# Kernel optimization log

Measured on AMD Instinct MI355X. Metric: run time of the kernel, lower is better.

Reference implementation:

```python
import jax, jax.numpy as jnp
import numpy as np

N_NODES = 100_000
N_EDGES = 1_600_000
F_IN = 128
NHID = 128
G = 64            # num graphs in the batch
N_CLASSES = 2
EMB = NHID * 6    # embedding_data dim so concat dim == NHID*8


def _lin_init(k, fi, fo):
    s = 1.0 / np.sqrt(fi)
    k1, k2 = jax.random.split(k)
    w = jax.random.uniform(k1, (fi, fo), jnp.float32, -s, s)
    b = jax.random.uniform(k2, (fo,), jnp.float32, -s, s)
    return w, b


def setup_inputs() -> dict:
    key = jax.random.key(0)
    ks = jax.random.split(key, 12)
    x = jax.random.normal(ks[0], (N_NODES, F_IN), jnp.float32)
    edge_index = jax.random.randint(ks[1], (2, N_EDGES), 0, N_NODES, dtype=jnp.int32)
    per = N_NODES // G
    batch = jnp.minimum(jnp.arange(N_NODES, dtype=jnp.int32) // per, G - 1)  # sorted, even split
    embedding_data = jax.random.normal(ks[2], (G, EMB), jnp.float32)
    conv_w, conv_b = _lin_init(ks[3], F_IN, NHID)
    lin0_w, lin0_b = _lin_init(ks[4], F_IN, NHID)
    lin1_w, lin1_b = _lin_init(ks[5], NHID * 8, NHID * 4)
    lin2_w, lin2_b = _lin_init(ks[6], NHID * 4, NHID * 2)
    lin3_w, lin3_b = _lin_init(ks[7], NHID * 2, NHID)
    lin4_w, lin4_b = _lin_init(ks[8], NHID, N_CLASSES)
    return {
        "x": x, "embedding_data": embedding_data,
        "conv_w": conv_w, "conv_b": conv_b,
        "lin0_w": lin0_w, "lin0_b": lin0_b,
        "lin1_w": lin1_w, "lin1_b": lin1_b,
        "lin2_w": lin2_w, "lin2_b": lin2_b,
        "lin3_w": lin3_w, "lin3_b": lin3_b,
        "lin4_w": lin4_w, "lin4_b": lin4_b,
        "edge_index": edge_index, "batch": batch,
    }


def _gcn_conv(x, edge_index, w, b):
    """PyG GCNConv: add self-loops, symmetric deg^-1/2 normalization, linear, scatter-add."""
    n = x.shape[0]
    loop = jnp.arange(n, dtype=edge_index.dtype)
    src = jnp.concatenate([edge_index[0], loop])
    dst = jnp.concatenate([edge_index[1], loop])
    deg = jax.ops.segment_sum(jnp.ones_like(dst, dtype=x.dtype), dst, num_segments=n)
    dinv = jnp.where(deg > 0, jax.lax.rsqrt(deg), 0.0)
    norm = dinv[src] * dinv[dst]                     # [E+N]
    h = x @ w                                        # [N, NHID]
    msg = h[src] * norm[:, None]                     # gather  [E+N, NHID]
    out = jax.ops.segment_sum(msg, dst, num_segments=n)  # scatter-add
    return out + b


def reference(x, embedding_data, conv_w, conv_b, lin0_w, lin0_b,
              lin1_w, lin1_b, lin2_w, lin2_b, lin3_w, lin3_b,
              lin4_w, lin4_b, edge_index, batch):
    h = jax.nn.relu(_gcn_conv(x, edge_index, conv_w, conv_b))   # [N, NHID]
    pooled = jax.ops.segment_max(h, batch, num_segments=G)      # global max pool [G, NHID]
    # first node of each graph (batch is sorted)
    first_idx = jnp.searchsorted(batch, jnp.arange(G, dtype=batch.dtype))
    news = jax.nn.relu(x[first_idx] @ lin0_w + lin0_b)          # [G, NHID]
    z = jnp.concatenate([pooled, news, embedding_data], axis=1) # [G, NHID*8]
    z = jnp.tanh(z @ lin1_w + lin1_b)   # dropout = identity (eval mode)
    z = jnp.tanh(z @ lin2_w + lin2_b)
    z = jnp.tanh(z @ lin3_w + lin3_b)
    return jax.nn.log_softmax(z @ lin4_w + lin4_b, axis=-1)     # [G, N_CLASSES]
```

## Files before the change

kernel.cpp:

```cpp
#include <hip/hip_runtime.h>
#include <hip/hip_bf16.h>

#define N_NODES 100000
#define N_EDGES 1600000
#define F 128
#define G 64
#define EMB 768
#define PER 1562
#define CAP 96
#define NBUCK 256
#define BNODES 391
#define TILE 8192
#define NBIN 196
#define SLOT 80
#define GEMM_GRID 512
#define EWS_ENT 104

typedef __hip_bfloat16 bf16;
typedef __attribute__((ext_vector_type(8))) short short8;
typedef __attribute__((ext_vector_type(4))) float f32x4;
typedef unsigned int u32;

__device__ __forceinline__ float b2f(bf16 v) { return __bfloat162float(v); }
__device__ __forceinline__ short f2bs(float v) {
    bf16 b = __float2bfloat16(v);
    return *reinterpret_cast<short*>(&b);
}
__device__ __forceinline__ float bl16(u32 v) { return __uint_as_float(v << 16); }
__device__ __forceinline__ float bh16(u32 v) { return __uint_as_float(v & 0xffff0000u); }

__global__ void k_init(float* __restrict__ pooled) {
    int i = blockIdx.x * 256 + threadIdx.x;
    if (i < G * F) pooled[i] = 0.0f;
}

__global__ __launch_bounds__(256) void k_fat(const int* __restrict__ ei,
                                             int* __restrict__ cntarr,
                                             u32* __restrict__ stage,
                                             const float* __restrict__ x,
                                             const float* __restrict__ w,
                                             bf16* __restrict__ h) {
    int t = threadIdx.x;
    if (blockIdx.x < NBIN) {
        __shared__ int offs[NBUCK];
        offs[t] = 0;
        __syncthreads();
        int blk = blockIdx.x;
        int e0 = blk * TILE;
        int e1 = min(e0 + TILE, N_EDGES);
        for (int e = e0 + t; e < e1; e += 256) {
            int src = ei[e];
            int dst = ei[N_EDGES + e];
            int b = dst / BNODES;
            int dl = dst - b * BNODES;
            int pos = atomicAdd(&offs[b], 1);
            if (pos < SLOT)
                stage[((size_t)b * NBIN + blk) * SLOT + pos] = (u32)src | ((u32)dl << 17);
        }
        __syncthreads();
        cntarr[blk * NBUCK + t] = min(offs[t], SLOT);
    } else {
        __shared__ short wfrag[16384];
        for (int i = t; i < 16384; i += 256) {
            int j    = i & 7;
            int lane = (i >> 3) & 63;
            int kb   = (i >> 9) & 3;
            int ct   = i >> 11;
            int k    = kb * 32 + (lane >> 4) * 8 + j;
            int n    = ct * 16 + (lane & 15);
            wfrag[i] = f2bs(w[k * 128 + n]);
        }
        __syncthreads();

        int wv = t >> 6, lane = t & 63;
        int m = lane & 15, q = lane >> 4;
        int nchunks = (N_NODES + 63) / 64;
        for (int chunk = blockIdx.x - NBIN; chunk < nchunks; chunk += GEMM_GRID) {
            int row = chunk * 64 + wv * 16 + m;
            int rr = (row < N_NODES) ? row : 0;
            short8 a[4];
#pragma unroll
            for (int kb = 0; kb < 4; ++kb) {
                const float* src = x + (size_t)rr * F + kb * 32 + q * 8;
                float4 v0 = *(const float4*)src;
                float4 v1 = *(const float4*)(src + 4);
                short8 av;
                av[0] = f2bs(v0.x); av[1] = f2bs(v0.y); av[2] = f2bs(v0.z); av[3] = f2bs(v0.w);
                av[4] = f2bs(v1.x); av[5] = f2bs(v1.y); av[6] = f2bs(v1.z); av[7] = f2bs(v1.w);
                a[kb] = av;
            }
            f32x4 acc[8];
#pragma unroll
            for (int ct = 0; ct < 8; ++ct) {
                f32x4 c = {0.f, 0.f, 0.f, 0.f};
#pragma unroll
                for (int kb = 0; kb < 4; ++kb) {
                    short8 bfr = *(const short8*)&wfrag[((ct * 4 + kb) * 64 + lane) * 8];
                    c = __builtin_amdgcn_mfma_f32_16x16x32_bf16(a[kb], bfr, c, 0, 0, 0);
                }
                acc[ct] = c;
            }
            int rbase = chunk * 64 + wv * 16 + q * 4;
#pragma unroll
            for (int ct = 0; ct < 8; ++ct)
#pragma unroll
                for (int r = 0; r < 4; ++r) {
                    int ro = rbase + r;
                    if (ro < N_NODES) h[(size_t)ro * F + ct * 16 + m] = __float2bfloat16(acc[ct][r]);
                }
        }
    }
}

__global__ __launch_bounds__(1024) void k_scat(const u32* __restrict__ stage,
                                               const int* __restrict__ cntarr,
                                               int* __restrict__ cursor,
                                               float* __restrict__ dinv,
                                               int* __restrict__ slots) {
    __shared__ int lcur[BNODES];
    int b = blockIdx.x;
    int t = threadIdx.x;
    int wv = t >> 6, lane = t & 63;
    int nbase = b * BNODES;
    int bn = min(BNODES, N_NODES - nbase);
    if (bn <= 0) return;
    for (int l = t; l < bn; l += 1024) lcur[l] = 0;
    __syncthreads();
    for (int seg = wv; seg < NBIN; seg += 16) {
        int cnt = cntarr[seg * NBUCK + b];
        const u32* sp = stage + ((size_t)b * NBIN + seg) * SLOT;
        for (int i = lane; i < cnt; i += 64) {
            u32 p = sp[i];
            int src = (int)(p & 0x1FFFFu);
            int dl  = (int)(p >> 17);
            int pos = atomicAdd(&lcur[dl], 1);
            if (pos < CAP) slots[(size_t)(nbase + dl) * CAP + pos] = src;
        }
    }
    __syncthreads();
    for (int l = t; l < bn; l += 1024) {
        int c = lcur[l];
        cursor[nbase + l] = c;
        dinv[nbase + l] = rsqrtf((float)(c + 1));
    }
}

__global__ __launch_bounds__(256) void k_agg(const bf16* __restrict__ h,
                                             const float* __restrict__ dinv,
                                             const int* __restrict__ slots,
                                             const int* __restrict__ cnt,
                                             const float* __restrict__ cb,
                                             float* __restrict__ pooled) {
    __shared__ __align__(16) char smem[16 * EWS_ENT * 8];
    int2 (*ews)[EWS_ENT] = (int2(*)[EWS_ENT])smem;
    float (*red)[132] = (float(*)[132])smem;

    int t = threadIdx.x;
    int wv = t >> 6, lane = t & 63;
    int q  = lane >> 4;
    int fl = lane & 15;
    int nb = blockIdx.x * 16 + wv * 4;
    int node = nb + q;
    int row  = wv * 4 + q;

    int c0 = min(cnt[nb + 0], CAP), c1 = min(cnt[nb + 1], CAP);
    int c2 = min(cnt[nb + 2], CAP), c3 = min(cnt[nb + 3], CAP);
    int cq   = (q == 0) ? c0 : (q == 1) ? c1 : (q == 2) ? c2 : c3;
    int cmax = max(max(c0, c1), max(c2, c3));

    const int* slp = slots + (size_t)node * CAP;
#pragma unroll
    for (int k = 0; k < 7; ++k) {
        int j = k * 16 + fl;
        if (j < EWS_ENT) {
            int2 ew = {0, 0};
            if (j < cq) { int s = slp[j]; ew.x = s; ew.y = __float_as_int(dinv[s]); }
            ews[row][j] = ew;
        }
    }
    __syncthreads();

    float acc[8] = {0.f, 0.f, 0.f, 0.f, 0.f, 0.f, 0.f, 0.f};
    const uint4* ewv = (const uint4*)ews[row];
    const u32* hb = (const u32*)h;
    int fl4 = fl * 4;
    if (cmax > 0) {
        uint4 ea = ewv[0];
        uint4 eb = ewv[1];
        uint4 v0 = *(const uint4*)(hb + (size_t)ea.x * 64 + fl4);
        uint4 v1 = *(const uint4*)(hb + (size_t)ea.z * 64 + fl4);
        uint4 v2 = *(const uint4*)(hb + (size_t)eb.x * 64 + fl4);
        uint4 v3 = *(const uint4*)(hb + (size_t)eb.z * 64 + fl4);
        for (int s0 = 0; s0 < cmax; s0 += 4) {
            uint4 na = ewv[(s0 >> 1) + 2];
            uint4 nb4 = ewv[(s0 >> 1) + 3];
            uint4 n0 = *(const uint4*)(hb + (size_t)na.x * 64 + fl4);
            uint4 n1 = *(const uint4*)(hb + (size_t)na.z * 64 + fl4);
            uint4 n2 = *(const uint4*)(hb + (size_t)nb4.x * 64 + fl4);
            uint4 n3 = *(const uint4*)(hb + (size_t)nb4.z * 64 + fl4);
            float w0 = __uint_as_float(ea.y), w1 = __uint_as_float(ea.w);
            float w2 = __uint_as_float(eb.y), w3 = __uint_as_float(eb.w);
            acc[0] = fmaf(bl16(v0.x), w0, acc[0]);
            acc[1] = fmaf(bh16(v0.x), w0, acc[1]);
            acc[2] = fmaf(bl16(v0.y), w0, acc[2]);
            acc[3] = fmaf(bh16(v0.y), w0, acc[3]);
            acc[4] = fmaf(bl16(v0.z), w0, acc[4]);
            acc[5] = fmaf(bh16(v0.z), w0, acc[5]);
            acc[6] = fmaf(bl16(v0.w), w0, acc[6]);
            acc[7] = fmaf(bh16(v0.w), w0, acc[7]);
            acc[0] = fmaf(bl16(v1.x), w1, acc[0]);
            acc[1] = fmaf(bh16(v1.x), w1, acc[1]);
            acc[2] = fmaf(bl16(v1.y), w1, acc[2]);
            acc[3] = fmaf(bh16(v1.y), w1, acc[3]);
            acc[4] = fmaf(bl16(v1.z), w1, acc[4]);
            acc[5] = fmaf(bh16(v1.z), w1, acc[5]);
            acc[6] = fmaf(bl16(v1.w), w1, acc[6]);
            acc[7] = fmaf(bh16(v1.w), w1, acc[7]);
            acc[0] = fmaf(bl16(v2.x), w2, acc[0]);
            acc[1] = fmaf(bh16(v2.x), w2, acc[1]);
            acc[2] = fmaf(bl16(v2.y), w2, acc[2]);
            acc[3] = fmaf(bh16(v2.y), w2, acc[3]);
            acc[4] = fmaf(bl16(v2.z), w2, acc[4]);
            acc[5] = fmaf(bh16(v2.z), w2, acc[5]);
            acc[6] = fmaf(bl16(v2.w), w2, acc[6]);
            acc[7] = fmaf(bh16(v2.w), w2, acc[7]);
            acc[0] = fmaf(bl16(v3.x), w3, acc[0]);
            acc[1] = fmaf(bh16(v3.x), w3, acc[1]);
            acc[2] = fmaf(bl16(v3.y), w3, acc[2]);
            acc[3] = fmaf(bh16(v3.y), w3, acc[3]);
            acc[4] = fmaf(bl16(v3.z), w3, acc[4]);
            acc[5] = fmaf(bh16(v3.z), w3, acc[5]);
            acc[6] = fmaf(bl16(v3.w), w3, acc[6]);
            acc[7] = fmaf(bh16(v3.w), w3, acc[7]);
            ea = na; eb = nb4;
            v0 = n0; v1 = n1; v2 = n2; v3 = n3;
        }
    }

    float dn = dinv[node];
    float dn2 = dn * dn;
    uint4 hs = *(const uint4*)(hb + (size_t)node * 64 + fl4);
    float4 cbv0 = *(const float4*)&cb[8 * fl];
    float4 cbv1 = *(const float4*)&cb[8 * fl + 4];
    float s0v = fmaxf(fmaf(acc[0], dn, fmaf(bl16(hs.x), dn2, cbv0.x)), 0.f);
    float s1v = fmaxf(fmaf(acc[1], dn, fmaf(bh16(hs.x), dn2, cbv0.y)), 0.f);
    float s2v = fmaxf(fmaf(acc[2], dn, fmaf(bl16(hs.y), dn2, cbv0.z)), 0.f);
    float s3v = fmaxf(fmaf(acc[3], dn, fmaf(bh16(hs.y), dn2, cbv0.w)), 0.f);
    float s4v = fmaxf(fmaf(acc[4], dn, fmaf(bl16(hs.z), dn2, cbv1.x)), 0.f);
    float s5v = fmaxf(fmaf(acc[5], dn, fmaf(bh16(hs.z), dn2, cbv1.y)), 0.f);
    float s6v = fmaxf(fmaf(acc[6], dn, fmaf(bl16(hs.w), dn2, cbv1.z)), 0.f);
    float s7v = fmaxf(fmaf(acc[7], dn, fmaf(bh16(hs.w), dn2, cbv1.w)), 0.f);

    __syncthreads();
    *(float4*)&red[row][8 * fl]     = make_float4(s0v, s1v, s2v, s3v);
    *(float4*)&red[row][8 * fl + 4] = make_float4(s4v, s5v, s6v, s7v);
    __syncthreads();

    int n0 = blockIdx.x * 16;
    int g0 = min(n0 / PER, G - 1);
    int gL = min((n0 + 15) / PER, G - 1);
    if (g0 == gL) {
        if (wv == 0) {
            float m0 = red[0][2 * lane], m1 = red[0][2 * lane + 1];
#pragma unroll
            for (int r = 1; r < 16; ++r) {
                m0 = fmaxf(m0, red[r][2 * lane]);
                m1 = fmaxf(m1, red[r][2 * lane + 1]);
            }
            atomicMax((int*)&pooled[g0 * F + 2 * lane],     __float_as_int(m0));
            atomicMax((int*)&pooled[g0 * F + 2 * lane + 1], __float_as_int(m1));
        }
    } else {
#pragma unroll
        for (int r = 0; r < 4; ++r) {
            int rr = wv * 4 + r;
            int g = min((n0 + rr) / PER, G - 1);
            atomicMax((int*)&pooled[g * F + 2 * lane],     __float_as_int(red[rr][2 * lane]));
            atomicMax((int*)&pooled[g * F + 2 * lane + 1], __float_as_int(red[rr][2 * lane + 1]));
        }
    }
}

__global__ __launch_bounds__(256) void k_l1(const float* __restrict__ x,
                                            const float* __restrict__ pooled,
                                            const float* __restrict__ emb,
                                            const float* __restrict__ l0w,
                                            const float* __restrict__ l0b,
                                            const float* __restrict__ w1,
                                            const float* __restrict__ b1,
                                            float* __restrict__ z1) {
    int jc = blockIdx.x & 7;
    int g0 = (blockIdx.x >> 3) * 8;
    int t = threadIdx.x;
    __shared__ float zs[8][1024];
    __shared__ float xs[8][128];
    __shared__ float psum[4][8][64];
    for (int i = t; i < 8 * 128; i += 256) {
        int g = i >> 7, c = i & 127;
        zs[g][c] = pooled[(g0 + g) * 128 + c];
        xs[g][c] = x[(size_t)((g0 + g) * PER) * F + c];
    }
    for (int i = t; i < 8 * 768; i += 256) {
        int g = i / 768, c = i - g * 768;
        zs[g][256 + c] = emb[(g0 + g) * EMB + c];
    }
    __syncthreads();
    if (t < 128) {
        float nacc[8];
#pragma unroll
        for (int g = 0; g < 8; ++g) nacc[g] = l0b[t];
        for (int k = 0; k < 128; ++k) {
            float lw = l0w[k * 128 + t];
#pragma unroll
            for (int g = 0; g < 8; ++g) nacc[g] = fmaf(xs[g][k], lw, nacc[g]);
        }
#pragma unroll
        for (int g = 0; g < 8; ++g) zs[g][128 + t] = fmaxf(nacc[g], 0.f);
    }
    __syncthreads();
    int j = t & 63, kq = t >> 6;
    float acc[8] = {0.f, 0.f, 0.f, 0.f, 0.f, 0.f, 0.f, 0.f};
    const float* wp = w1 + (size_t)(kq * 256) * 512 + jc * 64 + j;
    for (int k = 0; k < 256; ++k) {
        float wv = wp[(size_t)k * 512];
        int kk = kq * 256 + k;
#pragma unroll
        for (int g = 0; g < 8; ++g) acc[g] = fmaf(zs[g][kk], wv, acc[g]);
    }
#pragma unroll
    for (int g = 0; g < 8; ++g) psum[kq][g][j] = acc[g];
    __syncthreads();
    for (int i = t; i < 512; i += 256) {
        int g = i >> 6, jj = i & 63;
        float s = b1[jc * 64 + jj] + psum[0][g][jj] + psum[1][g][jj]
                + psum[2][g][jj] + psum[3][g][jj];
        z1[(g0 + g) * 512 + jc * 64 + jj] = tanhf(s);
    }
}

__global__ __launch_bounds__(256) void k_l2(const float* __restrict__ z1,
                                            const float* __restrict__ w2,
                                            const float* __restrict__ b2,
                                            float* __restrict__ z2) {
    int jc = blockIdx.x & 3;
    int g0 = (blockIdx.x >> 2) * 8;
    int t = threadIdx.x;
    __shared__ float zs[8][512];
    __shared__ float psum[4][8][64];
    for (int i = t; i < 8 * 512; i += 256) {
        int g = i >> 9, c = i & 511;
        zs[g][c] = z1[(g0 + g) * 512 + c];
    }
    __syncthreads();
    int j = t & 63, kq = t >> 6;
    float acc[8] = {0.f, 0.f, 0.f, 0.f, 0.f, 0.f, 0.f, 0.f};
    const float* wp = w2 + (size_t)(kq * 128) * 256 + jc * 64 + j;
    for (int k = 0; k < 128; ++k) {
        float wv = wp[(size_t)k * 256];
        int kk = kq * 128 + k;
#pragma unroll
        for (int g = 0; g < 8; ++g) acc[g] = fmaf(zs[g][kk], wv, acc[g]);
    }
#pragma unroll
    for (int g = 0; g < 8; ++g) psum[kq][g][j] = acc[g];
    __syncthreads();
    for (int i = t; i < 512; i += 256) {
        int g = i >> 6, jj = i & 63;
        float s = b2[jc * 64 + jj] + psum[0][g][jj] + psum[1][g][jj]
                + psum[2][g][jj] + psum[3][g][jj];
        z2[(g0 + g) * 256 + jc * 64 + jj] = tanhf(s);
    }
}

__global__ __launch_bounds__(256) void k_l3out(const float* __restrict__ z2,
                                               const float* __restrict__ w3,
                                               const float* __restrict__ b3,
                                               const float* __restrict__ w4,
                                               const float* __restrict__ b4,
                                               float* __restrict__ out) {
    int g0 = blockIdx.x * 8;
    int t = threadIdx.x;
    __shared__ float zs[8][256];
    __shared__ float psum[2][8][128];
    __shared__ float z3s[8][128];
    __shared__ float logits[16];
    for (int i = t; i < 8 * 256; i += 256) {
        int g = i >> 8, c = i & 255;
        zs[g][c] = z2[(g0 + g) * 256 + c];
    }
    __syncthreads();
    int j = t & 127, kh = t >> 7;
    float acc[8] = {0.f, 0.f, 0.f, 0.f, 0.f, 0.f, 0.f, 0.f};
    const float* wp = w3 + (size_t)(kh * 128) * 128 + j;
    for (int k = 0; k < 128; ++k) {
        float wv = wp[(size_t)k * 128];
        int kk = kh * 128 + k;
#pragma unroll
        for (int g = 0; g < 8; ++g) acc[g] = fmaf(zs[g][kk], wv, acc[g]);
    }
#pragma unroll
    for (int g = 0; g < 8; ++g) psum[kh][g][j] = acc[g];
    __syncthreads();
    for (int i = t; i < 8 * 128; i += 256) {
        int g = i >> 7, jj = i & 127;
        z3s[g][jj] = tanhf(b3[jj] + psum[0][g][jj] + psum[1][g][jj]);
    }
    __syncthreads();
    if (t < 16) {
        int g = t >> 1, c = t & 1;
        float l = b4[c];
        for (int k = 0; k < 128; ++k) l += z3s[g][k] * w4[k * 2 + c];
        logits[t] = l;
    }
    __syncthreads();
    if (t < 8) {
        float l0 = logits[2 * t], l1 = logits[2 * t + 1];
        float m = fmaxf(l0, l1);
        float lse = m + logf(expf(l0 - m) + expf(l1 - m));
        out[(g0 + t) * 2 + 0] = l0 - lse;
        out[(g0 + t) * 2 + 1] = l1 - lse;
    }
}

extern "C" void kernel_launch(void* const* d_in, const int* in_sizes, int n_in,
                              void* d_out, int out_size, void* d_ws, size_t ws_size,
                              hipStream_t stream) {
    const float* x      = (const float*)d_in[0];
    const float* emb    = (const float*)d_in[1];
    const float* conv_w = (const float*)d_in[2];
    const float* conv_b = (const float*)d_in[3];
    const float* lin0_w = (const float*)d_in[4];
    const float* lin0_b = (const float*)d_in[5];
    const float* lin1_w = (const float*)d_in[6];
    const float* lin1_b = (const float*)d_in[7];
    const float* lin2_w = (const float*)d_in[8];
    const float* lin2_b = (const float*)d_in[9];
    const float* lin3_w = (const float*)d_in[10];
    const float* lin3_b = (const float*)d_in[11];
    const float* lin4_w = (const float*)d_in[12];
    const float* lin4_b = (const float*)d_in[13];
    const int*   ei     = (const int*)d_in[14];
    float* out = (float*)d_out;

    char* ws = (char*)d_ws;
    int*   cursor = (int*)ws;                         ws += (size_t)N_NODES * 4;
    float* dinv   = (float*)ws;                       ws += (size_t)N_NODES * 4;
    int*   slots  = (int*)ws;                         ws += (size_t)N_NODES * CAP * 4;
    bf16*  h      = (bf16*)ws;                        ws += (size_t)N_NODES * F * 2;
    float* pooled = (float*)ws;                       ws += (size_t)G * F * 4;
    int*   cntarr = (int*)ws;                         ws += (size_t)NBIN * NBUCK * 4;
    u32*   stage  = (u32*)ws;                         ws += (size_t)NBUCK * NBIN * SLOT * 4;
    float* z1     = (float*)ws;                       ws += (size_t)G * 512 * 4;
    float* z2     = (float*)ws;                       ws += (size_t)G * 256 * 4;

    k_init<<<(G * F + 255) / 256, 256, 0, stream>>>(pooled);
    k_fat<<<NBIN + GEMM_GRID, 256, 0, stream>>>(ei, cntarr, stage, x, conv_w, h);
    k_scat<<<NBUCK, 1024, 0, stream>>>(stage, cntarr, cursor, dinv, slots);
    k_agg<<<N_NODES / 16, 256, 0, stream>>>(h, dinv, slots, cursor, conv_b, pooled);
    k_l1<<<64, 256, 0, stream>>>(x, pooled, emb, lin0_w, lin0_b, lin1_w, lin1_b, z1);
    k_l2<<<32, 256, 0, stream>>>(z1, lin2_w, lin2_b, z2);
    k_l3out<<<8, 256, 0, stream>>>(z2, lin3_w, lin3_b, lin4_w, lin4_b, out);
}
```

Before: 306.3 us.

## Fuse all stages into one persistent cooperative kernel with grid syncs

Replaces the seven separate kernel launches with a single cooperative persistent kernel that runs binning, GEMM, scatter, aggregation and the MLP head as phases separated by grid-wide syncs. Grid size comes from an occupancy query, and the MLP stages are repartitioned into smaller per-block work units so more blocks share them. The goal is to remove launch gaps and the tail idle time between dependent kernels. The cost is grid-sync overhead, lower occupancy from 32 KB of shared memory per block, and fixed persistent-block scheduling in place of hardware block dispatch for the irregular aggregation.

```diff
diff --git a/kernel.cpp b/kernel.cpp
--- a/kernel.cpp
+++ b/kernel.cpp
@@ -1,5 +1,8 @@
 #include <hip/hip_runtime.h>
 #include <hip/hip_bf16.h>
+#include <hip/hip_cooperative_groups.h>
+
+namespace cg = cooperative_groups;
 
 #define N_NODES 100000
 #define N_EDGES 1600000
@@ -12,8 +15,10 @@
 #define BNODES 391
 #define TILE 8192
 #define NBIN 196
+#define HBIN 98
 #define SLOT 80
-#define GEMM_GRID 512
+#define NCHUNK 1563
+#define NAGG 6250
 #define EWS_ENT 104
 
 typedef __hip_bfloat16 bf16;
@@ -21,7 +26,6 @@
 typedef __attribute__((ext_vector_type(4))) float f32x4;
 typedef unsigned int u32;
 
-__device__ __forceinline__ float b2f(bf16 v) { return __bfloat162float(v); }
 __device__ __forceinline__ short f2bs(float v) {
     bf16 b = __float2bfloat16(v);
     return *reinterpret_cast<short*>(&b);
@@ -29,59 +33,72 @@
 __device__ __forceinline__ float bl16(u32 v) { return __uint_as_float(v << 16); }
 __device__ __forceinline__ float bh16(u32 v) { return __uint_as_float(v & 0xffff0000u); }
 
-__global__ void k_init(float* __restrict__ pooled) {
-    int i = blockIdx.x * 256 + threadIdx.x;
-    if (i < G * F) pooled[i] = 0.0f;
-}
-
-__global__ __launch_bounds__(256) void k_fat(const int* __restrict__ ei,
-                                             int* __restrict__ cntarr,
-                                             u32* __restrict__ stage,
-                                             const float* __restrict__ x,
-                                             const float* __restrict__ w,
-                                             bf16* __restrict__ h) {
+struct MegaArgs {
+    const int* ei; int* cntarr; u32* stage;
+    const float* x; const float* convw; bf16* h;
+    int* curB; int* curT; int* deg; float* dinv; int* slots;
+    const float* convb; float* pooled;
+    const float* emb; const float* l0w; const float* l0b;
+    const float* w1; const float* b1; float* z1;
+    const float* w2; const float* b2; float* z2;
+    const float* w3; const float* b3; const float* w4; const float* b4;
+    float* out;
+};
+
+__global__ __launch_bounds__(256) void mega(MegaArgs A) {
+    __shared__ __align__(16) char smem[32768];
+    cg::grid_group grid = cg::this_grid();
     int t = threadIdx.x;
-    if (blockIdx.x < NBIN) {
-        __shared__ int offs[NBUCK];
-        offs[t] = 0;
+    int wv = t >> 6, lane = t & 63;
+    int qq = lane >> 4, fl = lane & 15;
+    int nblk = (int)gridDim.x;
+    int tg = (int)blockIdx.x * 256 + t;
+    int tstride = nblk * 256;
+
+    for (int i = tg; i < N_NODES; i += tstride) { A.curB[i] = 0; A.curT[i] = 0; }
+    for (int i = tg; i < G * F; i += tstride) A.pooled[i] = 0.f;
+
+    int nbin_blk = min(NBIN, nblk >> 1);
+    if ((int)blockIdx.x < nbin_blk) {
+        int* offs = (int*)smem;
+        for (int blk = blockIdx.x; blk < NBIN; blk += nbin_blk) {
+            offs[t] = 0;
+            __syncthreads();
+            int e0 = blk * TILE;
+            int e1 = min(e0 + TILE, N_EDGES);
+            for (int e = e0 + t; e < e1; e += 256) {
+                int src = A.ei[e];
+                int dst = A.ei[N_EDGES + e];
+                int b = dst / BNODES;
+                int dl = dst - b * BNODES;
+                int pos = atomicAdd(&offs[b], 1);
+                if (pos < SLOT)
+                    A.stage[((size_t)b * NBIN + blk) * SLOT + pos] = (u32)src | ((u32)dl << 17);
+            }
+            __syncthreads();
+            A.cntarr[blk * NBUCK + t] = min(offs[t], SLOT);
+            __syncthreads();
+        }
+    } else {
+        short* wfrag = (short*)smem;
+        for (int i = t; i < 16384; i += 256) {
+            int j  = i & 7;
+            int ln = (i >> 3) & 63;
+            int kb = (i >> 9) & 3;
+            int ct = i >> 11;
+            int k  = kb * 32 + (ln >> 4) * 8 + j;
+            int n  = ct * 16 + (ln & 15);
+            wfrag[i] = f2bs(A.convw[k * 128 + n]);
+        }
         __syncthreads();
-        int blk = blockIdx.x;
-        int e0 = blk * TILE;
-        int e1 = min(e0 + TILE, N_EDGES);
-        for (int e = e0 + t; e < e1; e += 256) {
-            int src = ei[e];
-            int dst = ei[N_EDGES + e];
-            int b = dst / BNODES;
-            int dl = dst - b * BNODES;
-            int pos = atomicAdd(&offs[b], 1);
-            if (pos < SLOT)
-                stage[((size_t)b * NBIN + blk) * SLOT + pos] = (u32)src | ((u32)dl << 17);
-        }
-        __syncthreads();
-        cntarr[blk * NBUCK + t] = min(offs[t], SLOT);
-    } else {
-        __shared__ short wfrag[16384];
-        for (int i = t; i < 16384; i += 256) {
-            int j    = i & 7;
-            int lane = (i >> 3) & 63;
-            int kb   = (i >> 9) & 3;
-            int ct   = i >> 11;
-            int k    = kb * 32 + (lane >> 4) * 8 + j;
-            int n    = ct * 16 + (lane & 15);
-            wfrag[i] = f2bs(w[k * 128 + n]);
-        }
-        __syncthreads();
-
-        int wv = t >> 6, lane = t & 63;
-        int m = lane & 15, q = lane >> 4;
-        int nchunks = (N_NODES + 63) / 64;
-        for (int chunk = blockIdx.x - NBIN; chunk < nchunks; chunk += GEMM_GRID) {
-            int row = chunk * 64 + wv * 16 + m;
-            int rr = (row < N_NODES) ? row : 0;
+        int gemmB = nblk - nbin_blk;
+        for (int chunk = (int)blockIdx.x - nbin_blk; chunk < NCHUNK; chunk += gemmB) {
+            int row0 = chunk * 64 + wv * 16 + fl;
+            int rr = (row0 < N_NODES) ? row0 : 0;
             short8 a[4];
 #pragma unroll
             for (int kb = 0; kb < 4; ++kb) {
-                const float* src = x + (size_t)rr * F + kb * 32 + q * 8;
+                const float* src = A.x + (size_t)rr * F + kb * 32 + qq * 8;
                 float4 v0 = *(const float4*)src;
                 float4 v1 = *(const float4*)(src + 4);
                 short8 av;
@@ -100,364 +117,362 @@
                 }
                 acc[ct] = c;
             }
-            int rbase = chunk * 64 + wv * 16 + q * 4;
+            int rbase = chunk * 64 + wv * 16 + qq * 4;
 #pragma unroll
             for (int ct = 0; ct < 8; ++ct)
 #pragma unroll
                 for (int r = 0; r < 4; ++r) {
                     int ro = rbase + r;
-                    if (ro < N_NODES) h[(size_t)ro * F + ct * 16 + m] = __float2bfloat16(acc[ct][r]);
-                }
-        }
-    }
-}
-
-__global__ __launch_bounds__(1024) void k_scat(const u32* __restrict__ stage,
-                                               const int* __restrict__ cntarr,
-                                               int* __restrict__ cursor,
-                                               float* __restrict__ dinv,
-                                               int* __restrict__ slots) {
-    __shared__ int lcur[BNODES];
-    int b = blockIdx.x;
-    int t = threadIdx.x;
-    int wv = t >> 6, lane = t & 63;
-    int nbase = b * BNODES;
-    int bn = min(BNODES, N_NODES - nbase);
-    if (bn <= 0) return;
-    for (int l = t; l < bn; l += 1024) lcur[l] = 0;
-    __syncthreads();
-    for (int seg = wv; seg < NBIN; seg += 16) {
-        int cnt = cntarr[seg * NBUCK + b];
-        const u32* sp = stage + ((size_t)b * NBIN + seg) * SLOT;
-        for (int i = lane; i < cnt; i += 64) {
-            u32 p = sp[i];
-            int src = (int)(p & 0x1FFFFu);
-            int dl  = (int)(p >> 17);
-            int pos = atomicAdd(&lcur[dl], 1);
-            if (pos < CAP) slots[(size_t)(nbase + dl) * CAP + pos] = src;
-        }
-    }
-    __syncthreads();
-    for (int l = t; l < bn; l += 1024) {
-        int c = lcur[l];
-        cursor[nbase + l] = c;
-        dinv[nbase + l] = rsqrtf((float)(c + 1));
-    }
-}
-
-__global__ __launch_bounds__(256) void k_agg(const bf16* __restrict__ h,
-                                             const float* __restrict__ dinv,
-                                             const int* __restrict__ slots,
-                                             const int* __restrict__ cnt,
-                                             const float* __restrict__ cb,
-                                             float* __restrict__ pooled) {
-    __shared__ __align__(16) char smem[16 * EWS_ENT * 8];
-    int2 (*ews)[EWS_ENT] = (int2(*)[EWS_ENT])smem;
-    float (*red)[132] = (float(*)[132])smem;
-
-    int t = threadIdx.x;
-    int wv = t >> 6, lane = t & 63;
-    int q  = lane >> 4;
-    int fl = lane & 15;
-    int nb = blockIdx.x * 16 + wv * 4;
-    int node = nb + q;
-    int row  = wv * 4 + q;
-
-    int c0 = min(cnt[nb + 0], CAP), c1 = min(cnt[nb + 1], CAP);
-    int c2 = min(cnt[nb + 2], CAP), c3 = min(cnt[nb + 3], CAP);
-    int cq   = (q == 0) ? c0 : (q == 1) ? c1 : (q == 2) ? c2 : c3;
-    int cmax = max(max(c0, c1), max(c2, c3));
-
-    const int* slp = slots + (size_t)node * CAP;
-#pragma unroll
-    for (int k = 0; k < 7; ++k) {
-        int j = k * 16 + fl;
-        if (j < EWS_ENT) {
-            int2 ew = {0, 0};
-            if (j < cq) { int s = slp[j]; ew.x = s; ew.y = __float_as_int(dinv[s]); }
-            ews[row][j] = ew;
-        }
-    }
-    __syncthreads();
-
-    float acc[8] = {0.f, 0.f, 0.f, 0.f, 0.f, 0.f, 0.f, 0.f};
-    const uint4* ewv = (const uint4*)ews[row];
-    const u32* hb = (const u32*)h;
-    int fl4 = fl * 4;
-    if (cmax > 0) {
-        uint4 ea = ewv[0];
-        uint4 eb = ewv[1];
-        uint4 v0 = *(const uint4*)(hb + (size_t)ea.x * 64 + fl4);
-        uint4 v1 = *(const uint4*)(hb + (size_t)ea.z * 64 + fl4);
-        uint4 v2 = *(const uint4*)(hb + (size_t)eb.x * 64 + fl4);
-        uint4 v3 = *(const uint4*)(hb + (size_t)eb.z * 64 + fl4);
-        for (int s0 = 0; s0 < cmax; s0 += 4) {
-            uint4 na = ewv[(s0 >> 1) + 2];
-            uint4 nb4 = ewv[(s0 >> 1) + 3];
-            uint4 n0 = *(const uint4*)(hb + (size_t)na.x * 64 + fl4);
-            uint4 n1 = *(const uint4*)(hb + (size_t)na.z * 64 + fl4);
-            uint4 n2 = *(const uint4*)(hb + (size_t)nb4.x * 64 + fl4);
-            uint4 n3 = *(const uint4*)(hb + (size_t)nb4.z * 64 + fl4);
-            float w0 = __uint_as_float(ea.y), w1 = __uint_as_float(ea.w);
-            float w2 = __uint_as_float(eb.y), w3 = __uint_as_float(eb.w);
-            acc[0] = fmaf(bl16(v0.x), w0, acc[0]);
-            acc[1] = fmaf(bh16(v0.x), w0, acc[1]);
-            acc[2] = fmaf(bl16(v0.y), w0, acc[2]);
-            acc[3] = fmaf(bh16(v0.y), w0, acc[3]);
-            acc[4] = fmaf(bl16(v0.z), w0, acc[4]);
-            acc[5] = fmaf(bh16(v0.z), w0, acc[5]);
-            acc[6] = fmaf(bl16(v0.w), w0, acc[6]);
-            acc[7] = fmaf(bh16(v0.w), w0, acc[7]);
-            acc[0] = fmaf(bl16(v1.x), w1, acc[0]);
-            acc[1] = fmaf(bh16(v1.x), w1, acc[1]);
-            acc[2] = fmaf(bl16(v1.y), w1, acc[2]);
-            acc[3] = fmaf(bh16(v1.y), w1, acc[3]);
-            acc[4] = fmaf(bl16(v1.z), w1, acc[4]);
-            acc[5] = fmaf(bh16(v1.z), w1, acc[5]);
-            acc[6] = fmaf(bl16(v1.w), w1, acc[6]);
-            acc[7] = fmaf(bh16(v1.w), w1, acc[7]);
-            acc[0] = fmaf(bl16(v2.x), w2, acc[0]);
-            acc[1] = fmaf(bh16(v2.x), w2, acc[1]);
-            acc[2] = fmaf(bl16(v2.y), w2, acc[2]);
-            acc[3] = fmaf(bh16(v2.y), w2, acc[3]);
-            acc[4] = fmaf(bl16(v2.z), w2, acc[4]);
-            acc[5] = fmaf(bh16(v2.z), w2, acc[5]);
-            acc[6] = fmaf(bl16(v2.w), w2, acc[6]);
-            acc[7] = fmaf(bh16(v2.w), w2, acc[7]);
-            acc[0] = fmaf(bl16(v3.x), w3, acc[0]);
-            acc[1] = fmaf(bh16(v3.x), w3, acc[1]);
-            acc[2] = fmaf(bl16(v3.y), w3, acc[2]);
-            acc[3] = fmaf(bh16(v3.y), w3, acc[3]);
-            acc[4] = fmaf(bl16(v3.z), w3, acc[4]);
-            acc[5] = fmaf(bh16(v3.z), w3, acc[5]);
-            acc[6] = fmaf(bl16(v3.w), w3, acc[6]);
-            acc[7] = fmaf(bh16(v3.w), w3, acc[7]);
-            ea = na; eb = nb4;
-            v0 = n0; v1 = n1; v2 = n2; v3 = n3;
-        }
-    }
-
-    float dn = dinv[node];
-    float dn2 = dn * dn;
-    uint4 hs = *(const uint4*)(hb + (size_t)node * 64 + fl4);
-    float4 cbv0 = *(const float4*)&cb[8 * fl];
-    float4 cbv1 = *(const float4*)&cb[8 * fl + 4];
-    float s0v = fmaxf(fmaf(acc[0], dn, fmaf(bl16(hs.x), dn2, cbv0.x)), 0.f);
-    float s1v = fmaxf(fmaf(acc[1], dn, fmaf(bh16(hs.x), dn2, cbv0.y)), 0.f);
-    float s2v = fmaxf(fmaf(acc[2], dn, fmaf(bl16(hs.y), dn2, cbv0.z)), 0.f);
-    float s3v = fmaxf(fmaf(acc[3], dn, fmaf(bh16(hs.y), dn2, cbv0.w)), 0.f);
-    float s4v = fmaxf(fmaf(acc[4], dn, fmaf(bl16(hs.z), dn2, cbv1.x)), 0.f);
-    float s5v = fmaxf(fmaf(acc[5], dn, fmaf(bh16(hs.z), dn2, cbv1.y)), 0.f);
-    float s6v = fmaxf(fmaf(acc[6], dn, fmaf(bl16(hs.w), dn2, cbv1.z)), 0.f);
-    float s7v = fmaxf(fmaf(acc[7], dn, fmaf(bh16(hs.w), dn2, cbv1.w)), 0.f);
-
-    __syncthreads();
-    *(float4*)&red[row][8 * fl]     = make_float4(s0v, s1v, s2v, s3v);
-    *(float4*)&red[row][8 * fl + 4] = make_float4(s4v, s5v, s6v, s7v);
-    __syncthreads();
-
-    int n0 = blockIdx.x * 16;
-    int g0 = min(n0 / PER, G - 1);
-    int gL = min((n0 + 15) / PER, G - 1);
-    if (g0 == gL) {
-        if (wv == 0) {
-            float m0 = red[0][2 * lane], m1 = red[0][2 * lane + 1];
-#pragma unroll
-            for (int r = 1; r < 16; ++r) {
-                m0 = fmaxf(m0, red[r][2 * lane]);
-                m1 = fmaxf(m1, red[r][2 * lane + 1]);
-            }
-            atomicMax((int*)&pooled[g0 * F + 2 * lane],     __float_as_int(m0));
-            atomicMax((int*)&pooled[g0 * F + 2 * lane + 1], __float_as_int(m1));
-        }
-    } else {
-#pragma unroll
-        for (int r = 0; r < 4; ++r) {
-            int rr = wv * 4 + r;
-            int g = min((n0 + rr) / PER, G - 1);
-            atomicMax((int*)&pooled[g * F + 2 * lane],     __float_as_int(red[rr][2 * lane]));
-            atomicMax((int*)&pooled[g * F + 2 * lane + 1], __float_as_int(red[rr][2 * lane + 1]));
-        }
-    }
-}
-
-__global__ __launch_bounds__(256) void k_l1(const float* __restrict__ x,
-                                            const float* __restrict__ pooled,
-                                            const float* __restrict__ emb,
-                                            const float* __restrict__ l0w,
-                                            const float* __restrict__ l0b,
-                                            const float* __restrict__ w1,
-                                            const float* __restrict__ b1,
-                                            float* __restrict__ z1) {
-    int jc = blockIdx.x & 7;
-    int g0 = (blockIdx.x >> 3) * 8;
-    int t = threadIdx.x;
-    __shared__ float zs[8][1024];
-    __shared__ float xs[8][128];
-    __shared__ float psum[4][8][64];
-    for (int i = t; i < 8 * 128; i += 256) {
-        int g = i >> 7, c = i & 127;
-        zs[g][c] = pooled[(g0 + g) * 128 + c];
-        xs[g][c] = x[(size_t)((g0 + g) * PER) * F + c];
-    }
-    for (int i = t; i < 8 * 768; i += 256) {
-        int g = i / 768, c = i - g * 768;
-        zs[g][256 + c] = emb[(g0 + g) * EMB + c];
-    }
-    __syncthreads();
-    if (t < 128) {
-        float nacc[8];
-#pragma unroll
-        for (int g = 0; g < 8; ++g) nacc[g] = l0b[t];
-        for (int k = 0; k < 128; ++k) {
-            float lw = l0w[k * 128 + t];
-#pragma unroll
-            for (int g = 0; g < 8; ++g) nacc[g] = fmaf(xs[g][k], lw, nacc[g]);
-        }
-#pragma unroll
-        for (int g = 0; g < 8; ++g) zs[g][128 + t] = fmaxf(nacc[g], 0.f);
-    }
-    __syncthreads();
-    int j = t & 63, kq = t >> 6;
-    float acc[8] = {0.f, 0.f, 0.f, 0.f, 0.f, 0.f, 0.f, 0.f};
-    const float* wp = w1 + (size_t)(kq * 256) * 512 + jc * 64 + j;
-    for (int k = 0; k < 256; ++k) {
-        float wv = wp[(size_t)k * 512];
-        int kk = kq * 256 + k;
-#pragma unroll
-        for (int g = 0; g < 8; ++g) acc[g] = fmaf(zs[g][kk], wv, acc[g]);
-    }
-#pragma unroll
-    for (int g = 0; g < 8; ++g) psum[kq][g][j] = acc[g];
-    __syncthreads();
-    for (int i = t; i < 512; i += 256) {
-        int g = i >> 6, jj = i & 63;
-        float s = b1[jc * 64 + jj] + psum[0][g][jj] + psum[1][g][jj]
-                + psum[2][g][jj] + psum[3][g][jj];
-        z1[(g0 + g) * 512 + jc * 64 + jj] = tanhf(s);
-    }
-}
-
-__global__ __launch_bounds__(256) void k_l2(const float* __restrict__ z1,
-                                            const float* __restrict__ w2,
-                                            const float* __restrict__ b2,
-                                            float* __restrict__ z2) {
-    int jc = blockIdx.x & 3;
-    int g0 = (blockIdx.x >> 2) * 8;
-    int t = threadIdx.x;
-    __shared__ float zs[8][512];
-    __shared__ float psum[4][8][64];
-    for (int i = t; i < 8 * 512; i += 256) {
-        int g = i >> 9, c = i & 511;
-        zs[g][c] = z1[(g0 + g) * 512 + c];
-    }
-    __syncthreads();
-    int j = t & 63, kq = t >> 6;
-    float acc[8] = {0.f, 0.f, 0.f, 0.f, 0.f, 0.f, 0.f, 0.f};
-    const float* wp = w2 + (size_t)(kq * 128) * 256 + jc * 64 + j;
-    for (int k = 0; k < 128; ++k) {
-        float wv = wp[(size_t)k * 256];
-        int kk = kq * 128 + k;
-#pragma unroll
-        for (int g = 0; g < 8; ++g) acc[g] = fmaf(zs[g][kk], wv, acc[g]);
-    }
-#pragma unroll
-    for (int g = 0; g < 8; ++g) psum[kq][g][j] = acc[g];
-    __syncthreads();
-    for (int i = t; i < 512; i += 256) {
-        int g = i >> 6, jj = i & 63;
-        float s = b2[jc * 64 + jj] + psum[0][g][jj] + psum[1][g][jj]
-                + psum[2][g][jj] + psum[3][g][jj];
-        z2[(g0 + g) * 256 + jc * 64 + jj] = tanhf(s);
-    }
-}
-
-__global__ __launch_bounds__(256) void k_l3out(const float* __restrict__ z2,
-                                               const float* __restrict__ w3,
-                                               const float* __restrict__ b3,
-                                               const float* __restrict__ w4,
-                                               const float* __restrict__ b4,
-                                               float* __restrict__ out) {
-    int g0 = blockIdx.x * 8;
-    int t = threadIdx.x;
-    __shared__ float zs[8][256];
-    __shared__ float psum[2][8][128];
-    __shared__ float z3s[8][128];
-    __shared__ float logits[16];
-    for (int i = t; i < 8 * 256; i += 256) {
-        int g = i >> 8, c = i & 255;
-        zs[g][c] = z2[(g0 + g) * 256 + c];
-    }
-    __syncthreads();
-    int j = t & 127, kh = t >> 7;
-    float acc[8] = {0.f, 0.f, 0.f, 0.f, 0.f, 0.f, 0.f, 0.f};
-    const float* wp = w3 + (size_t)(kh * 128) * 128 + j;
-    for (int k = 0; k < 128; ++k) {
-        float wv = wp[(size_t)k * 128];
-        int kk = kh * 128 + k;
-#pragma unroll
-        for (int g = 0; g < 8; ++g) acc[g] = fmaf(zs[g][kk], wv, acc[g]);
-    }
-#pragma unroll
-    for (int g = 0; g < 8; ++g) psum[kh][g][j] = acc[g];
-    __syncthreads();
-    for (int i = t; i < 8 * 128; i += 256) {
-        int g = i >> 7, jj = i & 127;
-        z3s[g][jj] = tanhf(b3[jj] + psum[0][g][jj] + psum[1][g][jj]);
-    }
-    __syncthreads();
-    if (t < 16) {
-        int g = t >> 1, c = t & 1;
-        float l = b4[c];
-        for (int k = 0; k < 128; ++k) l += z3s[g][k] * w4[k * 2 + c];
-        logits[t] = l;
-    }
-    __syncthreads();
-    if (t < 8) {
-        float l0 = logits[2 * t], l1 = logits[2 * t + 1];
-        float m = fmaxf(l0, l1);
-        float lse = m + logf(expf(l0 - m) + expf(l1 - m));
-        out[(g0 + t) * 2 + 0] = l0 - lse;
-        out[(g0 + t) * 2 + 1] = l1 - lse;
+                    if (ro < N_NODES) A.h[(size_t)ro * F + ct * 16 + fl] = __float2bfloat16(acc[ct][r]);
+                }
+        }
+    }
+    grid.sync();
+
+    {
+        int* lcnt = (int*)smem;
+        for (int hb = blockIdx.x; hb < 2 * NBUCK; hb += nblk) {
+            int b = hb >> 1, half = hb & 1;
+            for (int s = t; s < HBIN; s += 256)
+                lcnt[s] = A.cntarr[(half * HBIN + s) * NBUCK + b];
+            __syncthreads();
+            for (int s = wv; s < HBIN; s += 4) {
+                int cv = lcnt[s];
+                const u32* sp = A.stage + ((size_t)b * NBIN + half * HBIN + s) * SLOT;
+                for (int i = lane; i < cv; i += 64) {
+                    u32 p = sp[i];
+                    int src = (int)(p & 0x1FFFFu);
+                    int dl  = (int)(p >> 17);
+                    int node = b * BNODES + dl;
+                    if (half == 0) {
+                        int pos = atomicAdd(&A.curB[node], 1);
+                        if (pos < CAP) A.slots[(size_t)node * CAP + pos] = src;
+                    } else {
+                        int pos = atomicAdd(&A.curT[node], 1);
+                        int ix = CAP - 1 - pos;
+                        if (ix >= 0) A.slots[(size_t)node * CAP + ix] = src;
+                    }
+                }
+            }
+            __syncthreads();
+        }
+    }
+    grid.sync();
+
+    for (int n = tg; n < N_NODES; n += tstride) {
+        int r = A.curB[n] + A.curT[n];
+        A.deg[n] = r;
+        A.dinv[n] = rsqrtf((float)(r + 1));
+    }
+    grid.sync();
+
+    {
+        int2 (*ews)[EWS_ENT] = (int2(*)[EWS_ENT])smem;
+        float (*red)[132] = (float(*)[132])smem;
+        const u32* hb32 = (const u32*)A.h;
+        for (int vb = blockIdx.x; vb < NAGG; vb += nblk) {
+            int nb = vb * 16 + wv * 4;
+            int node = nb + qq;
+            int row = wv * 4 + qq;
+
+            int c0 = min(A.deg[nb + 0], CAP), c1 = min(A.deg[nb + 1], CAP);
+            int c2 = min(A.deg[nb + 2], CAP), c3 = min(A.deg[nb + 3], CAP);
+            int cq = (qq == 0) ? c0 : (qq == 1) ? c1 : (qq == 2) ? c2 : c3;
+            int cmax = max(max(c0, c1), max(c2, c3));
+            int cbq = min(A.curB[node], CAP);
+
+            const int* slp = A.slots + (size_t)node * CAP;
+#pragma unroll
+            for (int k = 0; k < 7; ++k) {
+                int j = k * 16 + fl;
+                if (j < EWS_ENT) {
+                    int2 ew = {0, 0};
+                    if (j < cq) {
+                        int ix = (j < cbq) ? j : (CAP - 1 - (j - cbq));
+                        int s = slp[ix];
+                        ew.x = s; ew.y = __float_as_int(A.dinv[s]);
+                    }
+                    ews[row][j] = ew;
+                }
+            }
+            __syncthreads();
+
+            float acc[8] = {0.f, 0.f, 0.f, 0.f, 0.f, 0.f, 0.f, 0.f};
+            const uint4* ewv = (const uint4*)ews[row];
+            int fl4 = fl * 4;
+            if (cmax > 0) {
+                uint4 ea = ewv[0];
+                uint4 eb = ewv[1];
+                uint4 v0 = *(const uint4*)(hb32 + (size_t)ea.x * 64 + fl4);
+                uint4 v1 = *(const uint4*)(hb32 + (size_t)ea.z * 64 + fl4);
+                uint4 v2 = *(const uint4*)(hb32 + (size_t)eb.x * 64 + fl4);
+                uint4 v3 = *(const uint4*)(hb32 + (size_t)eb.z * 64 + fl4);
+                for (int s0 = 0; s0 < cmax; s0 += 4) {
+                    uint4 na = ewv[(s0 >> 1) + 2];
+                    uint4 nb4 = ewv[(s0 >> 1) + 3];
+                    uint4 n0 = *(const uint4*)(hb32 + (size_t)na.x * 64 + fl4);
+                    uint4 n1 = *(const uint4*)(hb32 + (size_t)na.z * 64 + fl4);
+                    uint4 n2 = *(const uint4*)(hb32 + (size_t)nb4.x * 64 + fl4);
+                    uint4 n3 = *(const uint4*)(hb32 + (size_t)nb4.z * 64 + fl4);
+                    float w0 = __uint_as_float(ea.y), w1 = __uint_as_float(ea.w);
+                    float w2 = __uint_as_float(eb.y), w3 = __uint_as_float(eb.w);
+                    acc[0] = fmaf(bl16(v0.x), w0, acc[0]);
+                    acc[1] = fmaf(bh16(v0.x), w0, acc[1]);
+                    acc[2] = fmaf(bl16(v0.y), w0, acc[2]);
+                    acc[3] = fmaf(bh16(v0.y), w0, acc[3]);
+                    acc[4] = fmaf(bl16(v0.z), w0, acc[4]);
+                    acc[5] = fmaf(bh16(v0.z), w0, acc[5]);
+                    acc[6] = fmaf(bl16(v0.w), w0, acc[6]);
+                    acc[7] = fmaf(bh16(v0.w), w0, acc[7]);
+                    acc[0] = fmaf(bl16(v1.x), w1, acc[0]);
+                    acc[1] = fmaf(bh16(v1.x), w1, acc[1]);
+                    acc[2] = fmaf(bl16(v1.y), w1, acc[2]);
+                    acc[3] = fmaf(bh16(v1.y), w1, acc[3]);
+                    acc[4] = fmaf(bl16(v1.z), w1, acc[4]);
+                    acc[5] = fmaf(bh16(v1.z), w1, acc[5]);
+                    acc[6] = fmaf(bl16(v1.w), w1, acc[6]);
+                    acc[7] = fmaf(bh16(v1.w), w1, acc[7]);
+                    acc[0] = fmaf(bl16(v2.x), w2, acc[0]);
+                    acc[1] = fmaf(bh16(v2.x), w2, acc[1]);
+                    acc[2] = fmaf(bl16(v2.y), w2, acc[2]);
+                    acc[3] = fmaf(bh16(v2.y), w2, acc[3]);
+                    acc[4] = fmaf(bl16(v2.z), w2, acc[4]);
+                    acc[5] = fmaf(bh16(v2.z), w2, acc[5]);
+                    acc[6] = fmaf(bl16(v2.w), w2, acc[6]);
+                    acc[7] = fmaf(bh16(v2.w), w2, acc[7]);
+                    acc[0] = fmaf(bl16(v3.x), w3, acc[0]);
+                    acc[1] = fmaf(bh16(v3.x), w3, acc[1]);
+                    acc[2] = fmaf(bl16(v3.y), w3, acc[2]);
+                    acc[3] = fmaf(bh16(v3.y), w3, acc[3]);
+                    acc[4] = fmaf(bl16(v3.z), w3, acc[4]);
+                    acc[5] = fmaf(bh16(v3.z), w3, acc[5]);
+                    acc[6] = fmaf(bl16(v3.w), w3, acc[6]);
+                    acc[7] = fmaf(bh16(v3.w), w3, acc[7]);
+                    ea = na; eb = nb4;
+                    v0 = n0; v1 = n1; v2 = n2; v3 = n3;
+                }
+            }
+
+            float dn = A.dinv[node];
+            float dn2 = dn * dn;
+            uint4 hs = *(const uint4*)(hb32 + (size_t)node * 64 + fl4);
+            float4 cbv0 = *(const float4*)&A.convb[8 * fl];
+            float4 cbv1 = *(const float4*)&A.convb[8 * fl + 4];
+            float s0v = fmaxf(fmaf(acc[0], dn, fmaf(bl16(hs.x), dn2, cbv0.x)), 0.f);
+            float s1v = fmaxf(fmaf(acc[1], dn, fmaf(bh16(hs.x), dn2, cbv0.y)), 0.f);
+            float s2v = fmaxf(fmaf(acc[2], dn, fmaf(bl16(hs.y), dn2, cbv0.z)), 0.f);
+            float s3v = fmaxf(fmaf(acc[3], dn, fmaf(bh16(hs.y), dn2, cbv0.w)), 0.f);
+            float s4v = fmaxf(fmaf(acc[4], dn, fmaf(bl16(hs.z), dn2, cbv1.x)), 0.f);
+            float s5v = fmaxf(fmaf(acc[5], dn, fmaf(bh16(hs.z), dn2, cbv1.y)), 0.f);
+            float s6v = fmaxf(fmaf(acc[6], dn, fmaf(bl16(hs.w), dn2, cbv1.z)), 0.f);
+            float s7v = fmaxf(fmaf(acc[7], dn, fmaf(bh16(hs.w), dn2, cbv1.w)), 0.f);
+
+            __syncthreads();
+            *(float4*)&red[row][8 * fl]     = make_float4(s0v, s1v, s2v, s3v);
+            *(float4*)&red[row][8 * fl + 4] = make_float4(s4v, s5v, s6v, s7v);
+            __syncthreads();
+
+            int n0i = vb * 16;
+            int g0 = min(n0i / PER, G - 1);
+            int gL = min((n0i + 15) / PER, G - 1);
+            if (g0 == gL) {
+                if (wv == 0) {
+                    float m0 = red[0][2 * lane], m1 = red[0][2 * lane + 1];
+#pragma unroll
+                    for (int r = 1; r < 16; ++r) {
+                        m0 = fmaxf(m0, red[r][2 * lane]);
+                        m1 = fmaxf(m1, red[r][2 * lane + 1]);
+                    }
+                    atomicMax((int*)&A.pooled[g0 * F + 2 * lane],     __float_as_int(m0));
+                    atomicMax((int*)&A.pooled[g0 * F + 2 * lane + 1], __float_as_int(m1));
+                }
+            } else {
+#pragma unroll
+                for (int r = 0; r < 4; ++r) {
+                    int rr = wv * 4 + r;
+                    int g = min((n0i + rr) / PER, G - 1);
+                    atomicMax((int*)&A.pooled[g * F + 2 * lane],     __float_as_int(red[rr][2 * lane]));
+                    atomicMax((int*)&A.pooled[g * F + 2 * lane + 1], __float_as_int(red[rr][2 * lane + 1]));
+                }
+            }
+            __syncthreads();
+        }
+    }
+    grid.sync();
+
+    {
+        float (*zs)[1024] = (float(*)[1024])smem;
+        float (*xs)[128]  = (float(*)[128])(smem + 8192);
+        float (*ps)[2][64] = (float(*)[2][64])(smem + 9216);
+        for (int vb = blockIdx.x; vb < 256; vb += nblk) {
+            int jc = vb & 7;
+            int g0 = (vb >> 3) * 2;
+            for (int i = t; i < 2 * 128; i += 256) {
+                int g = i >> 7, c = i & 127;
+                zs[g][c] = A.pooled[(g0 + g) * 128 + c];
+                xs[g][c] = A.x[(size_t)((g0 + g) * PER) * F + c];
+            }
+            for (int i = t; i < 2 * 768; i += 256) {
+                int g = i / 768, c = i - g * 768;
+                zs[g][256 + c] = A.emb[(g0 + g) * EMB + c];
+            }
+            __syncthreads();
+            if (t < 128) {
+                float n0a = A.l0b[t], n1a = A.l0b[t];
+                for (int k = 0; k < 128; ++k) {
+                    float lw = A.l0w[k * 128 + t];
+                    n0a = fmaf(xs[0][k], lw, n0a);
+                    n1a = fmaf(xs[1][k], lw, n1a);
+                }
+                zs[0][128 + t] = fmaxf(n0a, 0.f);
+                zs[1][128 + t] = fmaxf(n1a, 0.f);
+            }
+            __syncthreads();
+            int j = t & 63, kq = t >> 6;
+            float a0 = 0.f, a1 = 0.f;
+            const float* wp = A.w1 + (size_t)(kq * 256) * 512 + jc * 64 + j;
+            for (int k = 0; k < 256; ++k) {
+                float wv1 = wp[(size_t)k * 512];
+                int kk = kq * 256 + k;
+                a0 = fmaf(zs[0][kk], wv1, a0);
+                a1 = fmaf(zs[1][kk], wv1, a1);
+            }
+            ps[kq][0][j] = a0; ps[kq][1][j] = a1;
+            __syncthreads();
+            for (int i = t; i < 128; i += 256) {
+                int g = i >> 6, jj = i & 63;
+                float s = A.b1[jc * 64 + jj] + ps[0][g][jj] + ps[1][g][jj]
+                        + ps[2][g][jj] + ps[3][g][jj];
+                A.z1[(g0 + g) * 512 + jc * 64 + jj] = tanhf(s);
+            }
+            __syncthreads();
+        }
+    }
+    grid.sync();
+
+    {
+        float (*zs)[512] = (float(*)[512])smem;
+        float (*ps)[4][64] = (float(*)[4][64])(smem + 8192);
+        for (int vb = blockIdx.x; vb < 64; vb += nblk) {
+            int jc = vb & 3;
+            int g0 = (vb >> 2) * 4;
+            for (int i = t; i < 4 * 512; i += 256) {
+                int g = i >> 9, c = i & 511;
+                zs[g][c] = A.z1[(g0 + g) * 512 + c];
+            }
+            __syncthreads();
+            int j = t & 63, kq = t >> 6;
+            float acc[4] = {0.f, 0.f, 0.f, 0.f};
+            const float* wp = A.w2 + (size_t)(kq * 128) * 256 + jc * 64 + j;
+            for (int k = 0; k < 128; ++k) {
+                float wv2 = wp[(size_t)k * 256];
+                int kk = kq * 128 + k;
+#pragma unroll
+                for (int g = 0; g < 4; ++g) acc[g] = fmaf(zs[g][kk], wv2, acc[g]);
+            }
+#pragma unroll
+            for (int g = 0; g < 4; ++g) ps[kq][g][j] = acc[g];
+            __syncthreads();
+            for (int i = t; i < 256; i += 256) {
+                int g = i >> 6, jj = i & 63;
+                float s = A.b2[jc * 64 + jj] + ps[0][g][jj] + ps[1][g][jj]
+                        + ps[2][g][jj] + ps[3][g][jj];
+                A.z2[(g0 + g) * 256 + jc * 64 + jj] = tanhf(s);
+            }
+            __syncthreads();
+        }
+    }
+    grid.sync();
+
+    {
+        float (*zs)[256] = (float(*)[256])smem;
+        float (*ps)[8][128] = (float(*)[8][128])(smem + 8192);
+        float (*z3s)[128] = (float(*)[128])(smem + 16384);
+        float* logits = (float*)(smem + 20480);
+        for (int vb = blockIdx.x; vb < 8; vb += nblk) {
+            int g0 = vb * 8;
+            for (int i = t; i < 8 * 256; i += 256) {
+                int g = i >> 8, c = i & 255;
+                zs[g][c] = A.z2[(g0 + g) * 256 + c];
+            }
+            __syncthreads();
+            int j = t & 127, kh = t >> 7;
+            float acc[8] = {0.f, 0.f, 0.f, 0.f, 0.f, 0.f, 0.f, 0.f};
+            const float* wp = A.w3 + (size_t)(kh * 128) * 128 + j;
+            for (int k = 0; k < 128; ++k) {
+                float wv3 = wp[(size_t)k * 128];
+                int kk = kh * 128 + k;
+#pragma unroll
+                for (int g = 0; g < 8; ++g) acc[g] = fmaf(zs[g][kk], wv3, acc[g]);
+            }
+#pragma unroll
+            for (int g = 0; g < 8; ++g) ps[kh][g][j] = acc[g];
+            __syncthreads();
+            for (int i = t; i < 8 * 128; i += 256) {
+                int g = i >> 7, jj = i & 127;
+                z3s[g][jj] = tanhf(A.b3[jj] + ps[0][g][jj] + ps[1][g][jj]);
+            }
+            __syncthreads();
+            if (t < 16) {
+                int g = t >> 1, c = t & 1;
+                float l = A.b4[c];
+                for (int k = 0; k < 128; ++k) l += z3s[g][k] * A.w4[k * 2 + c];
+                logits[t] = l;
+            }
+            __syncthreads();
+            if (t < 8) {
+                float l0 = logits[2 * t], l1 = logits[2 * t + 1];
+                float m = fmaxf(l0, l1);
+                float lse = m + logf(expf(l0 - m) + expf(l1 - m));
+                A.out[(g0 + t) * 2 + 0] = l0 - lse;
+                A.out[(g0 + t) * 2 + 1] = l1 - lse;
+            }
+            __syncthreads();
+        }
     }
 }
 
 extern "C" void kernel_launch(void* const* d_in, const int* in_sizes, int n_in,
                               void* d_out, int out_size, void* d_ws, size_t ws_size,
                               hipStream_t stream) {
-    const float* x      = (const float*)d_in[0];
-    const float* emb    = (const float*)d_in[1];
-    const float* conv_w = (const float*)d_in[2];
-    const float* conv_b = (const float*)d_in[3];
-    const float* lin0_w = (const float*)d_in[4];
-    const float* lin0_b = (const float*)d_in[5];
-    const float* lin1_w = (const float*)d_in[6];
-    const float* lin1_b = (const float*)d_in[7];
-    const float* lin2_w = (const float*)d_in[8];
-    const float* lin2_b = (const float*)d_in[9];
-    const float* lin3_w = (const float*)d_in[10];
-    const float* lin3_b = (const float*)d_in[11];
-    const float* lin4_w = (const float*)d_in[12];
-    const float* lin4_b = (const float*)d_in[13];
-    const int*   ei     = (const int*)d_in[14];
-    float* out = (float*)d_out;
+    MegaArgs A;
+    A.x      = (const float*)d_in[0];
+    A.emb    = (const float*)d_in[1];
+    A.convw  = (const float*)d_in[2];
+    A.convb  = (const float*)d_in[3];
+    A.l0w    = (const float*)d_in[4];
+    A.l0b    = (const float*)d_in[5];
+    A.w1     = (const float*)d_in[6];
+    A.b1     = (const float*)d_in[7];
+    A.w2     = (const float*)d_in[8];
+    A.b2     = (const float*)d_in[9];
+    A.w3     = (const float*)d_in[10];
+    A.b3     = (const float*)d_in[11];
+    A.w4     = (const float*)d_in[12];
+    A.b4     = (const float*)d_in[13];
+    A.ei     = (const int*)d_in[14];
+    A.out = (float*)d_out;
 
     char* ws = (char*)d_ws;
-    int*   cursor = (int*)ws;                         ws += (size_t)N_NODES * 4;
-    float* dinv   = (float*)ws;                       ws += (size_t)N_NODES * 4;
-    int*   slots  = (int*)ws;                         ws += (size_t)N_NODES * CAP * 4;
-    bf16*  h      = (bf16*)ws;                        ws += (size_t)N_NODES * F * 2;
-    float* pooled = (float*)ws;                       ws += (size_t)G * F * 4;
-    int*   cntarr = (int*)ws;                         ws += (size_t)NBIN * NBUCK * 4;
-    u32*   stage  = (u32*)ws;                         ws += (size_t)NBUCK * NBIN * SLOT * 4;
-    float* z1     = (float*)ws;                       ws += (size_t)G * 512 * 4;
-    float* z2     = (float*)ws;                       ws += (size_t)G * 256 * 4;
-
-    k_init<<<(G * F + 255) / 256, 256, 0, stream>>>(pooled);
-    k_fat<<<NBIN + GEMM_GRID, 256, 0, stream>>>(ei, cntarr, stage, x, conv_w, h);
-    k_scat<<<NBUCK, 1024, 0, stream>>>(stage, cntarr, cursor, dinv, slots);
-    k_agg<<<N_NODES / 16, 256, 0, stream>>>(h, dinv, slots, cursor, conv_b, pooled);
-    k_l1<<<64, 256, 0, stream>>>(x, pooled, emb, lin0_w, lin0_b, lin1_w, lin1_b, z1);
-    k_l2<<<32, 256, 0, stream>>>(z1, lin2_w, lin2_b, z2);
-    k_l3out<<<8, 256, 0, stream>>>(z2, lin3_w, lin3_b, lin4_w, lin4_b, out);
+    A.deg    = (int*)ws;                              ws += (size_t)N_NODES * 4;
+    A.dinv   = (float*)ws;                            ws += (size_t)N_NODES * 4;
+    A.slots  = (int*)ws;                              ws += (size_t)N_NODES * CAP * 4;
+    A.h      = (bf16*)ws;                             ws += (size_t)N_NODES * F * 2;
+    A.pooled = (float*)ws;                            ws += (size_t)G * F * 4;
+    A.cntarr = (int*)ws;                              ws += (size_t)NBIN * NBUCK * 4;
+    A.stage  = (u32*)ws;                              ws += (size_t)NBUCK * NBIN * SLOT * 4;
+    A.z1     = (float*)ws;                            ws += (size_t)G * 512 * 4;
+    A.z2     = (float*)ws;                            ws += (size_t)G * 256 * 4;
+    A.curB   = (int*)ws;                              ws += (size_t)N_NODES * 4;
+    A.curT   = (int*)ws;                              ws += (size_t)N_NODES * 4;
+
+    static int nblk = 0;
+    if (nblk == 0) {
+        int occ = 0;
+        if (hipOccupancyMaxActiveBlocksPerMultiprocessor(&occ, mega, 256, 0) != hipSuccess || occ < 1)
+            occ = 2;
+        nblk = occ * 256;
+    }
+    void* args[] = { (void*)&A };
+    hipLaunchCooperativeKernel((const void*)mega, dim3(nblk), dim3(256), args, 0, stream);
 }
```

Result: slower. 609.6 us (+99.1%).
